# Optimization experiments

Hardware: AMD Instinct MI355X
Metric: run time of the kernel (lower is better)

The kernel has to match this reference:

```python
import jax, jax.numpy as jnp
import numpy as np

B, L, D, H, I = 4, 2048, 768, 12, 3072
HD = D // H  # 64
EPS = 1e-5


def _ln(x, g, b):
    mu = jnp.mean(x, axis=-1, keepdims=True)
    var = jnp.var(x, axis=-1, keepdims=True)
    return (x - mu) * jax.lax.rsqrt(var + EPS) * g + b


def setup_inputs() -> dict:
    key = jax.random.key(0)
    ks = jax.random.split(key, 8)
    s = 0.02
    return {
        "x": jax.random.normal(ks[0], (B, L, D), dtype=jnp.float32),
        "attention_mask": jnp.ones((B, L), dtype=bool),
        "ln1_g": jnp.ones((D,), jnp.float32),
        "ln1_b": jnp.zeros((D,), jnp.float32),
        "w_qkv": jax.random.normal(ks[1], (D, 3 * D), jnp.float32) * s,
        "b_qkv": jnp.zeros((3 * D,), jnp.float32),
        "w_o": jax.random.normal(ks[2], (D, D), jnp.float32) * s,
        "b_o": jnp.zeros((D,), jnp.float32),
        "ln2_g": jnp.ones((D,), jnp.float32),
        "ln2_b": jnp.zeros((D,), jnp.float32),
        "w1": jax.random.normal(ks[3], (D, I), jnp.float32) * s,
        "b1": jnp.zeros((I,), jnp.float32),
        "w2": jax.random.normal(ks[4], (I, D), jnp.float32) * s,
        "b2": jnp.zeros((D,), jnp.float32),
    }


def reference(x, attention_mask, ln1_g, ln1_b, w_qkv, b_qkv, w_o, b_o,
              ln2_g, ln2_b, w1, b1, w2, b2):
    # pre-LN + fused qkv projection
    h = _ln(x, ln1_g, ln1_b)
    qkv = h @ w_qkv + b_qkv                      # [B,L,3D]
    qkv = qkv.reshape(B, L, H, 3 * HD)           # chunk per-head: first HD=q, then k, then v
    q, k, v = qkv[..., :HD], qkv[..., HD:2 * HD], qkv[..., 2 * HD:]
    # NOTE: original divides by head_dim (q.size(-1)), NOT sqrt(head_dim)
    scores = jnp.einsum('blhd,bmhd->bhlm', q, k) / HD   # [B,H,L,L]
    causal = jnp.tril(jnp.ones((L, L), dtype=bool))
    full_mask = attention_mask[:, None, None, :] & causal
    scores = jnp.where(full_mask, scores, -jnp.inf)
    p = jax.nn.softmax(scores, axis=-1)
    attn = jnp.einsum('bhlm,bmhd->blhd', p, v).reshape(B, L, D)
    out_attn = attn @ w_o + b_o + x
    # FFN: Sequential(Linear, Linear, GELU, Dropout) -> GELU applied LAST (faithful to source)
    h2 = _ln(out_attn, ln2_g, ln2_b)
    ff = jax.nn.gelu((h2 @ w1 + b1) @ w2 + b2, approximate=False)
    return out_attn + ff
```

## Files before the change

### kernel.cpp

```cpp
#include <hip/hip_runtime.h>
#include <stdint.h>

typedef __attribute__((ext_vector_type(8))) short short8;
typedef __attribute__((ext_vector_type(4))) float f32x4;

typedef const void __attribute__((address_space(1)))* gas1_t;
typedef void __attribute__((address_space(3)))* las3_t;
#define GLL16(g, l) __builtin_amdgcn_global_load_lds((gas1_t)(const void*)(g), (las3_t)(void*)(l), 16, 0, 0)

__device__ __forceinline__ unsigned short f2bf(float x){
  union { float f; unsigned u; } c; c.f = x;
  return (unsigned short)((c.u + 0x7fffu + ((c.u >> 16) & 1u)) >> 16);
}
__device__ __forceinline__ float bf2f(unsigned short u){
  union { unsigned u; float f; } c; c.u = ((unsigned)u) << 16; return c.f;
}
__device__ __forceinline__ unsigned cvtpk(float lo, float hi){
  unsigned r;
  asm("v_cvt_pk_bf16_f32 %0, %1, %2" : "=v"(r) : "v"(lo), "v"(hi));
  return r;
}

constexpr int Bc = 4, Lc = 2048, Dc = 768, Hc = 12, HDc = 64, Ic = 3072;
constexpr int Mrows = Bc * Lc;
constexpr int N3 = 3 * Dc;

__global__ void transpose_w(const float* __restrict__ W, unsigned short* __restrict__ Wt, int K, int N){
  __shared__ float t[32][33];
  int n0 = blockIdx.x * 32, k0 = blockIdx.y * 32;
  int tx = threadIdx.x, ty = threadIdx.y;
  #pragma unroll
  for (int j = 0; j < 4; ++j)
    t[ty + 8*j][tx] = W[(size_t)(k0 + ty + 8*j) * N + n0 + tx];
  __syncthreads();
  #pragma unroll
  for (int j = 0; j < 4; ++j)
    Wt[(size_t)(n0 + ty + 8*j) * K + k0 + tx] = f2bf(t[tx][ty + 8*j]);
}

__global__ void transpose_v(const unsigned short* __restrict__ qkv, unsigned short* __restrict__ vt){
  __shared__ unsigned short t[32][33];
  int l0 = blockIdx.x * 32, d0 = blockIdx.y * 32;
  int bh = blockIdx.z; int b = bh / Hc, h = bh - b * Hc;
  int tx = threadIdx.x, ty = threadIdx.y;
  const unsigned short* src = qkv + (size_t)b * Lc * N3 + h * 192 + 128;
  #pragma unroll
  for (int j = 0; j < 4; ++j)
    t[ty + 8*j][tx] = src[(size_t)(l0 + ty + 8*j) * N3 + d0 + tx];
  __syncthreads();
  unsigned short* dst = vt + (size_t)bh * 64 * Lc;
  #pragma unroll
  for (int j = 0; j < 4; ++j)
    dst[(size_t)(d0 + ty + 8*j) * Lc + l0 + tx] = t[tx][ty + 8*j];
}

__global__ __launch_bounds__(256) void ln_kernel(const float* __restrict__ x, const float* __restrict__ g,
                                                 const float* __restrict__ bta, unsigned short* __restrict__ out){
  int row = blockIdx.x, tid = threadIdx.x;
  const float* xr = x + (size_t)row * 768;
  float v0 = xr[tid], v1 = xr[tid + 256], v2 = xr[tid + 512];
  float s = v0 + v1 + v2;
  float ss = v0*v0 + v1*v1 + v2*v2;
  #pragma unroll
  for (int o = 32; o > 0; o >>= 1){ s += __shfl_xor(s, o); ss += __shfl_xor(ss, o); }
  __shared__ float red[8];
  int w = tid >> 6;
  if ((tid & 63) == 0){ red[w] = s; red[4 + w] = ss; }
  __syncthreads();
  s  = red[0] + red[1] + red[2] + red[3];
  ss = red[4] + red[5] + red[6] + red[7];
  float mu  = s * (1.f / 768.f);
  float var = ss * (1.f / 768.f) - mu * mu;
  float rs  = rsqrtf(var + 1e-5f);
  unsigned short* orow = out + (size_t)row * 768;
  orow[tid]       = f2bf((v0 - mu) * rs * g[tid]       + bta[tid]);
  orow[tid + 256] = f2bf((v1 - mu) * rs * g[tid + 256] + bta[tid + 256]);
  orow[tid + 512] = f2bf((v2 - mu) * rs * g[tid + 512] + bta[tid + 512]);
}

__global__ __launch_bounds__(256) void ln_kernel_bf(const unsigned short* __restrict__ x, const float* __restrict__ g,
                                                    const float* __restrict__ bta, unsigned short* __restrict__ out){
  int row = blockIdx.x, tid = threadIdx.x;
  const unsigned short* xr = x + (size_t)row * 768;
  float v0 = bf2f(xr[tid]), v1 = bf2f(xr[tid + 256]), v2 = bf2f(xr[tid + 512]);
  float s = v0 + v1 + v2;
  float ss = v0*v0 + v1*v1 + v2*v2;
  #pragma unroll
  for (int o = 32; o > 0; o >>= 1){ s += __shfl_xor(s, o); ss += __shfl_xor(ss, o); }
  __shared__ float red[8];
  int w = tid >> 6;
  if ((tid & 63) == 0){ red[w] = s; red[4 + w] = ss; }
  __syncthreads();
  s  = red[0] + red[1] + red[2] + red[3];
  ss = red[4] + red[5] + red[6] + red[7];
  float mu  = s * (1.f / 768.f);
  float var = ss * (1.f / 768.f) - mu * mu;
  float rs  = rsqrtf(var + 1e-5f);
  unsigned short* orow = out + (size_t)row * 768;
  orow[tid]       = f2bf((v0 - mu) * rs * g[tid]       + bta[tid]);
  orow[tid + 256] = f2bf((v1 - mu) * rs * g[tid + 256] + bta[tid + 256]);
  orow[tid + 512] = f2bf((v2 - mu) * rs * g[tid + 512] + bta[tid + 512]);
}

template<int MODE>
__global__ __launch_bounds__(512, 4) void gemm_wide(
    const unsigned short* __restrict__ A, const unsigned short* __restrict__ Bt,
    const float* __restrict__ bias, const float* __restrict__ res,
    void* __restrict__ outp, int Kdim, int Ndim)
{
  __shared__ __align__(16) unsigned short Als[128 * 64];
  __shared__ __align__(16) unsigned short Bls[2][256 * 64];
  int tid = threadIdx.x, w = tid >> 6, lane = tid & 63;
  int g = lane >> 4, r16 = lane & 15;
  int wm = w >> 2, wn = w & 3;

  int nwg = gridDim.x * gridDim.y;
  int flat = blockIdx.y * gridDim.x + blockIdx.x;
  int cpx = nwg >> 3;
  int swz = (flat & 7) * cpx + (flat >> 3);
  int bx = swz % gridDim.x, by = swz / gridDim.x;
  int m0 = by * 128, n0 = bx * 256;

  f32x4 acc[4][4];
  #pragma unroll
  for (int m = 0; m < 4; ++m)
    #pragma unroll
    for (int n = 0; n < 4; ++n) acc[m][n] = f32x4{0.f, 0.f, 0.f, 0.f};

  int lrow = lane >> 3;
  int gsw8 = ((lane & 7) ^ lrow) * 8;
  auto stageA = [&](int kt){
    int k0 = kt * 64;
    #pragma unroll
    for (int i = 0; i < 2; ++i){
      int c = w * 2 + i;
      int row = c * 8 + lrow;
      GLL16(A + (size_t)(m0 + row) * Kdim + k0 + gsw8, &Als[c * 512]);
    }
  };
  auto stageB = [&](int buf, int kt){
    int k0 = kt * 64;
    #pragma unroll
    for (int i = 0; i < 4; ++i){
      int c = w * 4 + i;
      int row = c * 8 + lrow;
      GLL16(Bt + (size_t)(n0 + row) * Kdim + k0 + gsw8, &Bls[buf][c * 512]);
    }
  };

  int nk = Kdim >> 6;
  stageB(0, 0);
  int cur = 0;
  for (int kt = 0; kt < nk; ++kt){
    __builtin_amdgcn_s_barrier();
    stageA(kt);
    if (kt + 1 < nk){
      stageB(cur ^ 1, kt + 1);
      asm volatile("s_waitcnt vmcnt(4)" ::: "memory");
    } else {
      asm volatile("s_waitcnt vmcnt(0)" ::: "memory");
    }
    __builtin_amdgcn_s_barrier();

    #pragma unroll
    for (int ks = 0; ks < 2; ++ks){
      short8 af[4], bfv[4];
      #pragma unroll
      for (int m = 0; m < 4; ++m){
        int r = wm * 64 + m * 16 + r16;
        af[m] = *(const short8*)&Als[r * 64 + (((ks*4 + g) ^ (r & 7)) << 3)];
      }
      #pragma unroll
      for (int n = 0; n < 4; ++n){
        int r = wn * 64 + n * 16 + r16;
        bfv[n] = *(const short8*)&Bls[cur][r * 64 + (((ks*4 + g) ^ (r & 7)) << 3)];
      }
      __builtin_amdgcn_s_setprio(1);
      #pragma unroll
      for (int m = 0; m < 4; ++m)
        #pragma unroll
        for (int n = 0; n < 4; ++n)
          acc[m][n] = __builtin_amdgcn_mfma_f32_16x16x32_bf16(af[m], bfv[n], acc[m][n], 0, 0, 0);
      __builtin_amdgcn_s_setprio(0);
    }
    cur ^= 1;
  }

  #pragma unroll
  for (int n = 0; n < 4; ++n){
    int col = n0 + wn * 64 + n * 16 + r16;
    float bv = bias[col];
    #pragma unroll
    for (int m = 0; m < 4; ++m){
      #pragma unroll
      for (int j = 0; j < 4; ++j){
        int rowg = m0 + wm * 64 + m * 16 + g * 4 + j;
        size_t idx = (size_t)rowg * Ndim + col;
        float v = acc[m][n][j] + bv;
        ((unsigned short*)outp)[idx] = f2bf(v);
      }
    }
  }
}

template<int MODE>
__global__ __launch_bounds__(512, 6) void gemm64(
    const unsigned short* __restrict__ A, const unsigned short* __restrict__ Bt,
    const float* __restrict__ bias, const void* __restrict__ res,
    void* __restrict__ outp, int Kdim, int Ndim)
{
  __shared__ __align__(16) unsigned short Als[2][64 * 64];
  __shared__ __align__(16) unsigned short Bls[2][128 * 64];
  int tid = threadIdx.x, w = tid >> 6, lane = tid & 63;
  int g = lane >> 4, r16 = lane & 15;
  int wm = w >> 2, wn = w & 3;

  int nwg = gridDim.x * gridDim.y;
  int flat = blockIdx.y * gridDim.x + blockIdx.x;
  int cpx = nwg >> 3;
  int swz = (flat & 7) * cpx + (flat >> 3);
  int bx = swz % gridDim.x, by = swz / gridDim.x;
  int m0 = by * 64, n0 = bx * 128;

  f32x4 acc[2][2];
  #pragma unroll
  for (int m = 0; m < 2; ++m)
    #pragma unroll
    for (int n = 0; n < 2; ++n) acc[m][n] = f32x4{0.f, 0.f, 0.f, 0.f};

  int lrow = lane >> 3;
  int gsw8 = ((lane & 7) ^ lrow) * 8;
  auto stage = [&](int buf, int kt){
    int k0 = kt * 64;
    {
      int c = w;
      int row = c * 8 + lrow;
      GLL16(A + (size_t)(m0 + row) * Kdim + k0 + gsw8, &Als[buf][c * 512]);
    }
    #pragma unroll
    for (int i = 0; i < 2; ++i){
      int c = w * 2 + i;
      int row = c * 8 + lrow;
      GLL16(Bt + (size_t)(n0 + row) * Kdim + k0 + gsw8, &Bls[buf][c * 512]);
    }
  };

  int nk = Kdim >> 6;
  stage(0, 0);
  int cur = 0;
  for (int kt = 0; kt < nk; ++kt){
    __builtin_amdgcn_s_barrier();
    if (kt + 1 < nk){
      stage(cur ^ 1, kt + 1);
      asm volatile("s_waitcnt vmcnt(3)" ::: "memory");
    } else {
      asm volatile("s_waitcnt vmcnt(0)" ::: "memory");
    }
    __builtin_amdgcn_s_barrier();

    #pragma unroll
    for (int ks = 0; ks < 2; ++ks){
      short8 af[2], bfv[2];
      #pragma unroll
      for (int m = 0; m < 2; ++m){
        int r = wm * 32 + m * 16 + r16;
        af[m] = *(const short8*)&Als[cur][r * 64 + (((ks*4 + g) ^ (r & 7)) << 3)];
      }
      #pragma unroll
      for (int n = 0; n < 2; ++n){
        int r = wn * 32 + n * 16 + r16;
        bfv[n] = *(const short8*)&Bls[cur][r * 64 + (((ks*4 + g) ^ (r & 7)) << 3)];
      }
      #pragma unroll
      for (int m = 0; m < 2; ++m)
        #pragma unroll
        for (int n = 0; n < 2; ++n)
          acc[m][n] = __builtin_amdgcn_mfma_f32_16x16x32_bf16(af[m], bfv[n], acc[m][n], 0, 0, 0);
    }
    cur ^= 1;
  }

  #pragma unroll
  for (int n = 0; n < 2; ++n){
    int col = n0 + wn * 32 + n * 16 + r16;
    float bv = bias[col];
    #pragma unroll
    for (int m = 0; m < 2; ++m){
      #pragma unroll
      for (int j = 0; j < 4; ++j){
        int rowg = m0 + wm * 32 + m * 16 + g * 4 + j;
        size_t idx = (size_t)rowg * Ndim + col;
        float v = acc[m][n][j] + bv;
        if (MODE == 1){
          ((unsigned short*)outp)[idx] = f2bf(v + ((const float*)res)[idx]);
        } else {
          float ge = 0.5f * v * (1.0f + erff(v * 0.70710678118f));
          ((float*)outp)[idx] = bf2f(((const unsigned short*)res)[idx]) + ge;
        }
      }
    }
  }
}

__global__ __launch_bounds__(256, 3) void attn_kernel(const unsigned short* __restrict__ qkv,
                                                      const unsigned short* __restrict__ vt,
                                                      unsigned short* __restrict__ attn_out){
  int qt = 15 - blockIdx.y;
  int bh = blockIdx.x;
  int b = bh / Hc, h = bh - b * Hc;
  int tid = threadIdx.x, w = tid >> 6, lane = tid & 63;
  int g = lane >> 4, r16 = lane & 15;
  const unsigned short* base  = qkv + (size_t)b * Lc * N3 + h * 192;
  const unsigned short* vbase = vt + (size_t)bh * 64 * Lc;

  __shared__ __align__(16) unsigned short Kls[2][64 * 64];
  __shared__ __align__(16) unsigned short Vls[2][64 * 64];
  __shared__ __align__(16) unsigned short Pls[4][32 * 64];

  constexpr float SM_SCALE = 0.022542110013890052f;

  int qw = qt * 128 + w * 32;
  short8 qf[2][2];
  #pragma unroll
  for (int mq = 0; mq < 2; ++mq)
    #pragma unroll
    for (int dh = 0; dh < 2; ++dh){
      short8 v = *(const short8*)(base + (size_t)(qw + mq*16 + r16) * N3 + dh*32 + g*8);
      union { unsigned u[4]; short8 s8; } r;
      #pragma unroll
      for (int i = 0; i < 4; ++i){
        float lo = bf2f((unsigned short)v[2*i])     * SM_SCALE;
        float hi = bf2f((unsigned short)v[2*i + 1]) * SM_SCALE;
        r.u[i] = cvtpk(lo, hi);
      }
      qf[mq][dh] = r.s8;
    }

  short8 ones;
  #pragma unroll
  for (int i = 0; i < 8; ++i) ones[i] = (short)0x3F80;

  f32x4 o[2][4];
  f32x4 acc_l[2];
  #pragma unroll
  for (int mq = 0; mq < 2; ++mq){
    #pragma unroll
    for (int nd = 0; nd < 4; ++nd) o[mq][nd] = f32x4{0.f, 0.f, 0.f, 0.f};
    acc_l[mq] = f32x4{0.f, 0.f, 0.f, 0.f};
  }

  unsigned short* Pw = &Pls[w][0];

  int lrow = lane >> 3, csw8 = ((lane & 7) ^ lrow) * 8;
  auto stage = [&](int buf, int kt){
    #pragma unroll
    for (int i = 0; i < 2; ++i){
      int r0 = (w * 2 + i) * 8;
      int row = r0 + lrow;
      GLL16(base  + (size_t)(kt*64 + row) * N3 + 64 + csw8, &Kls[buf][r0 * 64]);
      GLL16(vbase + (size_t)row * Lc + kt*64 + csw8,        &Vls[buf][r0 * 64]);
    }
  };

  auto compute_tile = [&](int cur, int kt, bool diag){
    f32x4 s[2][4];
    #pragma unroll
    for (int mq = 0; mq < 2; ++mq)
      #pragma unroll
      for (int nk = 0; nk < 4; ++nk) s[mq][nk] = f32x4{0.f,0.f,0.f,0.f};
    #pragma unroll
    for (int nk = 0; nk < 4; ++nk){
      int krow = nk*16 + r16;
      #pragma unroll
      for (int dh = 0; dh < 2; ++dh){
        short8 kf = *(const short8*)&Kls[cur][krow * 64 + (((dh*4 + g) ^ (krow & 7)) << 3)];
        #pragma unroll
        for (int mq = 0; mq < 2; ++mq)
          s[mq][nk] = __builtin_amdgcn_mfma_f32_16x16x32_bf16(qf[mq][dh], kf, s[mq][nk], 0, 0, 0);
      }
    }
    #pragma unroll
    for (int mq = 0; mq < 2; ++mq){
      int qv = qw + mq*16 + g*4;
      #pragma unroll
      for (int nk = 0; nk < 4; ++nk){
        int kc = kt*64 + nk*16 + r16;
        #pragma unroll
        for (int j = 0; j < 4; ++j){
          float t = s[mq][nk][j];
          if (diag) t = (kc <= qv + j) ? t : -1e30f;
          float p = __builtin_amdgcn_exp2f(t);
          union { float f; unsigned u; } c; c.f = p;
          int row = mq*16 + g*4 + j, col = nk*16 + r16;
          Pw[(row << 6) + ((((col >> 3) ^ (row & 7)) << 3) | (col & 7))] =
              (unsigned short)((c.u + 0x8000u) >> 16);
        }
      }
    }
    asm volatile("" ::: "memory");
    short8 pf[2][2];
    #pragma unroll
    for (int mq = 0; mq < 2; ++mq){
      int prow = mq*16 + r16;
      #pragma unroll
      for (int ks = 0; ks < 2; ++ks)
        pf[mq][ks] = *(const short8*)&Pw[(prow << 6) + (((ks*4 + g) ^ (prow & 7)) << 3)];
      acc_l[mq] = __builtin_amdgcn_mfma_f32_16x16x32_bf16(pf[mq][0], ones, acc_l[mq], 0, 0, 0);
      acc_l[mq] = __builtin_amdgcn_mfma_f32_16x16x32_bf16(pf[mq][1], ones, acc_l[mq], 0, 0, 0);
    }
    #pragma unroll
    for (int ks = 0; ks < 2; ++ks){
      #pragma unroll
      for (int nd = 0; nd < 4; ++nd){
        int vrow = nd*16 + r16;
        short8 vf = *(const short8*)&Vls[cur][vrow * 64 + (((ks*4 + g) ^ (vrow & 7)) << 3)];
        #pragma unroll
        for (int mq = 0; mq < 2; ++mq)
          o[mq][nd] = __builtin_amdgcn_mfma_f32_16x16x32_bf16(pf[mq][ks], vf, o[mq][nd], 0, 0, 0);
      }
    }
  };

  int nkt = 2 * (qt + 1);
  stage(0, 0);
  __syncthreads();
  int cur = 0;
  for (int kt = 0; kt < nkt - 1; ++kt){
    stage(cur ^ 1, kt + 1);
    compute_tile(cur, kt, kt >= 2*qt);
    __syncthreads();
    cur ^= 1;
  }
  compute_tile(cur, nkt - 1, true);

  unsigned short* ob = attn_out + (size_t)b * Lc * Dc + h * HDc;
  #pragma unroll
  for (int mq = 0; mq < 2; ++mq){
    float inv[4];
    #pragma unroll
    for (int j = 0; j < 4; ++j) inv[j] = 1.0f / acc_l[mq][j];
    #pragma unroll
    for (int nd = 0; nd < 4; ++nd)
      #pragma unroll
      for (int j = 0; j < 4; ++j){
        int q2 = qw + mq*16 + g*4 + j;
        ob[(size_t)q2 * Dc + nd*16 + r16] = f2bf(o[mq][nd][j] * inv[j]);
      }
  }
}

extern "C" void kernel_launch(void* const* d_in, const int* in_sizes, int n_in,
                              void* d_out, int out_size, void* d_ws, size_t ws_size,
                              hipStream_t stream){
  const float* x     = (const float*)d_in[0];
  const float* ln1_g = (const float*)d_in[2];
  const float* ln1_b = (const float*)d_in[3];
  const float* w_qkv = (const float*)d_in[4];
  const float* b_qkv = (const float*)d_in[5];
  const float* w_o   = (const float*)d_in[6];
  const float* b_o   = (const float*)d_in[7];
  const float* ln2_g = (const float*)d_in[8];
  const float* ln2_b = (const float*)d_in[9];
  const float* w1    = (const float*)d_in[10];
  const float* b1    = (const float*)d_in[11];
  const float* w2    = (const float*)d_in[12];
  const float* b2    = (const float*)d_in[13];

  char* ws = (char*)d_ws;
  size_t off = 0;
  auto alloc = [&](size_t bytes){ void* p = ws + off; off += (bytes + 255) & ~(size_t)255; return p; };
  unsigned short* wqkv_t = (unsigned short*)alloc((size_t)N3 * Dc * 2);
  unsigned short* wo_t   = (unsigned short*)alloc((size_t)Dc * Dc * 2);
  unsigned short* w1_t   = (unsigned short*)alloc((size_t)Ic * Dc * 2);
  unsigned short* w2_t   = (unsigned short*)alloc((size_t)Dc * Ic * 2);
  unsigned short* hbuf   = (unsigned short*)alloc((size_t)Mrows * Dc * 2);
  unsigned short* oattn  = (unsigned short*)alloc((size_t)Mrows * Dc * 2);
  unsigned short* vtb    = (unsigned short*)alloc((size_t)Bc * Hc * HDc * Lc * 2);
  char*           big    = (char*)alloc((size_t)Mrows * Ic * 2);
  unsigned short* qkv    = (unsigned short*)big;
  unsigned short* attn_o = (unsigned short*)(big + (size_t)Mrows * N3 * 2);
  unsigned short* ff1    = (unsigned short*)big;

  dim3 tb(32, 8, 1);
  transpose_w<<<dim3(N3/32, Dc/32), tb, 0, stream>>>(w_qkv, wqkv_t, Dc, N3);
  transpose_w<<<dim3(Dc/32, Dc/32), tb, 0, stream>>>(w_o,   wo_t,   Dc, Dc);
  transpose_w<<<dim3(Ic/32, Dc/32), tb, 0, stream>>>(w1,    w1_t,   Dc, Ic);
  transpose_w<<<dim3(Dc/32, Ic/32), tb, 0, stream>>>(w2,    w2_t,   Ic, Dc);

  ln_kernel<<<dim3(Mrows), dim3(256), 0, stream>>>(x, ln1_g, ln1_b, hbuf);

  gemm_wide<0><<<dim3(N3/256, Mrows/128), dim3(512), 0, stream>>>(hbuf, wqkv_t, b_qkv, nullptr, (void*)qkv, Dc, N3);

  transpose_v<<<dim3(Lc/32, HDc/32, Bc*Hc), tb, 0, stream>>>(qkv, vtb);

  attn_kernel<<<dim3(Bc*Hc, Lc/128), dim3(256), 0, stream>>>(qkv, vtb, attn_o);

  gemm64<1><<<dim3(Dc/128, Mrows/64), dim3(512), 0, stream>>>(attn_o, wo_t, b_o, (const void*)x, (void*)oattn, Dc, Dc);

  ln_kernel_bf<<<dim3(Mrows), dim3(256), 0, stream>>>(oattn, ln2_g, ln2_b, hbuf);

  gemm_wide<0><<<dim3(Ic/256, Mrows/128), dim3(512), 0, stream>>>(hbuf, w1_t, b1, nullptr, (void*)ff1, Dc, Ic);

  gemm64<2><<<dim3(Dc/128, Mrows/64), dim3(512), 0, stream>>>(ff1, w2_t, b2, (const void*)oattn, d_out, Ic, Dc);
}
```

Measured before the change: 260.8 us.

## Restructure wide GEMM into double-buffered ping-pong pipeline with quadrant MFMA phases

Replaces the wide GEMM's main loop with a two-stage double-buffered pipeline for both A and B tiles. Each K-step is split into four quadrant MFMA phases separated by barriers, with the next tile's global-to-LDS loads issued between phases. The aim is to hide load latency and interleave LDS reads with MFMA work. In exchange it adds more barriers per iteration and raises LDS use to 96KB, which with launch bounds of 1 lowers occupancy. It assumes the K tile count is even.

```diff
diff --git a/kernel.cpp b/kernel.cpp
--- a/kernel.cpp
+++ b/kernel.cpp
@@ -102,13 +102,12 @@
   orow[tid + 512] = f2bf((v2 - mu) * rs * g[tid + 512] + bta[tid + 512]);
 }
 
-template<int MODE>
-__global__ __launch_bounds__(512, 4) void gemm_wide(
+__global__ __launch_bounds__(512, 1) void gemm8p(
     const unsigned short* __restrict__ A, const unsigned short* __restrict__ Bt,
-    const float* __restrict__ bias, const float* __restrict__ res,
-    void* __restrict__ outp, int Kdim, int Ndim)
+    const float* __restrict__ bias, unsigned short* __restrict__ outp,
+    int Kdim, int Ndim)
 {
-  __shared__ __align__(16) unsigned short Als[128 * 64];
+  __shared__ __align__(16) unsigned short Als[2][128 * 64];
   __shared__ __align__(16) unsigned short Bls[2][256 * 64];
   int tid = threadIdx.x, w = tid >> 6, lane = tid & 63;
   int g = lane >> 4, r16 = lane & 15;
@@ -129,13 +128,13 @@
 
   int lrow = lane >> 3;
   int gsw8 = ((lane & 7) ^ lrow) * 8;
-  auto stageA = [&](int kt){
+  auto stageA = [&](int buf, int kt){
     int k0 = kt * 64;
     #pragma unroll
     for (int i = 0; i < 2; ++i){
       int c = w * 2 + i;
       int row = c * 8 + lrow;
-      GLL16(A + (size_t)(m0 + row) * Kdim + k0 + gsw8, &Als[c * 512]);
+      GLL16(A + (size_t)(m0 + row) * Kdim + k0 + gsw8, &Als[buf][c * 512]);
     }
   };
   auto stageB = [&](int buf, int kt){
@@ -147,44 +146,85 @@
       GLL16(Bt + (size_t)(n0 + row) * Kdim + k0 + gsw8, &Bls[buf][c * 512]);
     }
   };
-
-  int nk = Kdim >> 6;
-  stageB(0, 0);
-  int cur = 0;
-  for (int kt = 0; kt < nk; ++kt){
-    __builtin_amdgcn_s_barrier();
-    stageA(kt);
-    if (kt + 1 < nk){
-      stageB(cur ^ 1, kt + 1);
-      asm volatile("s_waitcnt vmcnt(4)" ::: "memory");
-    } else {
-      asm volatile("s_waitcnt vmcnt(0)" ::: "memory");
-    }
-    __builtin_amdgcn_s_barrier();
-
-    #pragma unroll
-    for (int ks = 0; ks < 2; ++ks){
-      short8 af[4], bfv[4];
-      #pragma unroll
-      for (int m = 0; m < 4; ++m){
-        int r = wm * 64 + m * 16 + r16;
-        af[m] = *(const short8*)&Als[r * 64 + (((ks*4 + g) ^ (r & 7)) << 3)];
-      }
-      #pragma unroll
-      for (int n = 0; n < 4; ++n){
-        int r = wn * 64 + n * 16 + r16;
-        bfv[n] = *(const short8*)&Bls[cur][r * 64 + (((ks*4 + g) ^ (r & 7)) << 3)];
-      }
-      __builtin_amdgcn_s_setprio(1);
-      #pragma unroll
-      for (int m = 0; m < 4; ++m)
-        #pragma unroll
-        for (int n = 0; n < 4; ++n)
-          acc[m][n] = __builtin_amdgcn_mfma_f32_16x16x32_bf16(af[m], bfv[n], acc[m][n], 0, 0, 0);
-      __builtin_amdgcn_s_setprio(0);
-    }
-    cur ^= 1;
-  }
+  auto ldA = [&](int buf, int m, int ks) -> short8 {
+    int r = wm * 64 + m * 16 + r16;
+    return *(const short8*)&Als[buf][r * 64 + (((ks*4 + g) ^ (r & 7)) << 3)];
+  };
+  auto ldB = [&](int buf, int n, int ks) -> short8 {
+    int r = wn * 64 + n * 16 + r16;
+    return *(const short8*)&Bls[buf][r * 64 + (((ks*4 + g) ^ (r & 7)) << 3)];
+  };
+
+#define QMM(AF, BF, MB, NB) { \
+  __builtin_amdgcn_s_setprio(1); \
+  _Pragma("unroll") for (int m_ = 0; m_ < 2; ++m_) \
+  _Pragma("unroll") for (int n_ = 0; n_ < 2; ++n_) \
+  _Pragma("unroll") for (int k_ = 0; k_ < 2; ++k_) \
+    acc[(MB)+m_][(NB)+n_] = __builtin_amdgcn_mfma_f32_16x16x32_bf16(AF[m_][k_], BF[n_][k_], acc[(MB)+m_][(NB)+n_], 0, 0, 0); \
+  __builtin_amdgcn_s_setprio(0); }
+#define BAR() __builtin_amdgcn_s_barrier()
+
+  int NK = Kdim >> 6;
+  int NITER = NK >> 1;
+
+  stageB(0, 0); stageA(0, 0);
+  stageB(1, 1); stageA(1, 1);
+
+  short8 af[2][2], bf0[2][2], bf1[2][2];
+
+  for (int it = 0; it < NITER; ++it){
+    int t = 2 * it;
+    bool more = (t + 2 < NK);
+    bool last = (it == NITER - 1);
+
+    asm volatile("s_waitcnt vmcnt(6)" ::: "memory");
+    BAR();
+    #pragma unroll
+    for (int k_ = 0; k_ < 2; ++k_){
+      af[0][k_] = ldA(0, 0, k_); af[1][k_] = ldA(0, 1, k_);
+      bf0[0][k_] = ldB(0, 0, k_); bf0[1][k_] = ldB(0, 1, k_);
+    }
+    QMM(af, bf0, 0, 0);
+    BAR();
+    #pragma unroll
+    for (int k_ = 0; k_ < 2; ++k_){ bf1[0][k_] = ldB(0, 2, k_); bf1[1][k_] = ldB(0, 3, k_); }
+    QMM(af, bf1, 0, 2);
+    BAR();
+    #pragma unroll
+    for (int k_ = 0; k_ < 2; ++k_){ af[0][k_] = ldA(0, 2, k_); af[1][k_] = ldA(0, 3, k_); }
+    if (more) stageB(0, t + 2);
+    QMM(af, bf1, 2, 2);
+    BAR();
+    if (more) stageA(0, t + 2);
+    QMM(af, bf0, 2, 0);
+    BAR();
+
+    if (last) { asm volatile("s_waitcnt vmcnt(0)" ::: "memory"); }
+    else      { asm volatile("s_waitcnt vmcnt(6)" ::: "memory"); }
+    BAR();
+    #pragma unroll
+    for (int k_ = 0; k_ < 2; ++k_){
+      af[0][k_] = ldA(1, 0, k_); af[1][k_] = ldA(1, 1, k_);
+      bf0[0][k_] = ldB(1, 0, k_); bf0[1][k_] = ldB(1, 1, k_);
+    }
+    QMM(af, bf0, 0, 0);
+    BAR();
+    #pragma unroll
+    for (int k_ = 0; k_ < 2; ++k_){ bf1[0][k_] = ldB(1, 2, k_); bf1[1][k_] = ldB(1, 3, k_); }
+    QMM(af, bf1, 0, 2);
+    BAR();
+    #pragma unroll
+    for (int k_ = 0; k_ < 2; ++k_){ af[0][k_] = ldA(1, 2, k_); af[1][k_] = ldA(1, 3, k_); }
+    if (more) stageB(1, t + 3);
+    QMM(af, bf1, 2, 2);
+    BAR();
+    if (more) stageA(1, t + 3);
+    QMM(af, bf0, 2, 0);
+    BAR();
+  }
+
+#undef QMM
+#undef BAR
 
   #pragma unroll
   for (int n = 0; n < 4; ++n){
@@ -195,9 +235,7 @@
       #pragma unroll
       for (int j = 0; j < 4; ++j){
         int rowg = m0 + wm * 64 + m * 16 + g * 4 + j;
-        size_t idx = (size_t)rowg * Ndim + col;
-        float v = acc[m][n][j] + bv;
-        ((unsigned short*)outp)[idx] = f2bf(v);
+        outp[(size_t)rowg * Ndim + col] = f2bf(acc[m][n][j] + bv);
       }
     }
   }
@@ -489,7 +527,7 @@
 
   ln_kernel<<<dim3(Mrows), dim3(256), 0, stream>>>(x, ln1_g, ln1_b, hbuf);
 
-  gemm_wide<0><<<dim3(N3/256, Mrows/128), dim3(512), 0, stream>>>(hbuf, wqkv_t, b_qkv, nullptr, (void*)qkv, Dc, N3);
+  gemm8p<<<dim3(N3/256, Mrows/128), dim3(512), 0, stream>>>(hbuf, wqkv_t, b_qkv, qkv, Dc, N3);
 
   transpose_v<<<dim3(Lc/32, HDc/32, Bc*Hc), tb, 0, stream>>>(qkv, vtb);
 
@@ -499,7 +537,7 @@
 
   ln_kernel_bf<<<dim3(Mrows), dim3(256), 0, stream>>>(oattn, ln2_g, ln2_b, hbuf);
 
-  gemm_wide<0><<<dim3(Ic/256, Mrows/128), dim3(512), 0, stream>>>(hbuf, w1_t, b1, nullptr, (void*)ff1, Dc, Ic);
+  gemm8p<<<dim3(Ic/256, Mrows/128), dim3(512), 0, stream>>>(hbuf, w1_t, b1, ff1, Dc, Ic);
 
   gemm64<2><<<dim3(Dc/128, Mrows/64), dim3(512), 0, stream>>>(ff1, w2_t, b2, (const void*)oattn, d_out, Ic, Dc);
 }
```

Measured after the change: 275.9 us. 1.06x slower.
